# Kernel optimization log

Measured on AMD Instinct MI355X. Metric: run time of the kernel, lower is better.

Reference implementation:

```python
import jax, jax.numpy as jnp
import numpy as np

HC = 4            # hc_mult
HIDDEN = 4096
SINKHORN_ITERS = 5
HC_EPS = 1e-5
NORM_EPS = 1e-6
B, S = 2, 4096


def setup_inputs() -> dict:
    key = jax.random.key(0)
    k0, k1, k2, k3 = jax.random.split(key, 4)
    mix = (2 + HC) * HC  # 24
    return {
        "hidden_streams": jax.random.normal(k0, (B, S, HC, HIDDEN), dtype=jnp.float32),
        # small init so sigmoid/softmax gates stay in a sane range
        "fn": jax.random.normal(k1, (mix, HC * HIDDEN), dtype=jnp.float32) * 0.01,
        "base": jax.random.normal(k2, (mix,), dtype=jnp.float32),
        "scale": jax.random.normal(k3, (3,), dtype=jnp.float32),
    }


def reference(hidden_streams, fn, base, scale):
    hc = HC
    # flatten streams: [B, S, hc*hidden]
    flat = hidden_streams.reshape(hidden_streams.shape[0], hidden_streams.shape[1], -1).astype(jnp.float32)
    rsqrt = jax.lax.rsqrt(jnp.mean(jnp.square(flat), axis=-1, keepdims=True) + NORM_EPS)
    # packed projection to mix=(2+hc)*hc gate logits, RMS-scaled
    mix = jnp.einsum("bsd,md->bsm", flat, fn.astype(jnp.float32)) * rsqrt
    pre_scale, post_scale, comb_scale = scale[0], scale[1], scale[2]
    pre = jax.nn.sigmoid(mix[..., :hc] * pre_scale + base[:hc]) + HC_EPS
    post = 2.0 * jax.nn.sigmoid(mix[..., hc:2 * hc] * post_scale + base[hc:2 * hc])
    comb_logit = mix[..., 2 * hc:].reshape(*mix.shape[:-1], hc, hc) * comb_scale + base[2 * hc:].reshape(hc, hc)
    comb = jax.nn.softmax(comb_logit, axis=-1) + HC_EPS
    comb = comb / (jnp.sum(comb, axis=-2, keepdims=True) + HC_EPS)
    for _ in range(SINKHORN_ITERS - 1):
        comb = comb / (jnp.sum(comb, axis=-1, keepdims=True) + HC_EPS)
        comb = comb / (jnp.sum(comb, axis=-2, keepdims=True) + HC_EPS)
    return pre, post, comb
```

## Files before the change

### kernel.cpp

```cpp
#include <hip/hip_runtime.h>
#include <hip/hip_bf16.h>
#include <math.h>
#include <stdint.h>

#define HC 4
#define DIM 16384
#define MIXN 24
#define NROWS 8192
#define KSPLIT 16
#define KSL (DIM / KSPLIT)
#define NSTEPS (KSL / 32)
#define NSTREAM 32
#define ROWS_PER_STREAM (NROWS / NSTREAM)
#define THREADS1 512
#define NWAVE 8
#define ROWS_PER_BITER (NWAVE * 16)
#define NITER (ROWS_PER_STREAM / ROWS_PER_BITER)
#define HC_EPS 1e-5f
#define NORM_EPS 1e-6f

#define PRE_OFF 0
#define POST_OFF (NROWS * HC)
#define COMB_OFF (2 * NROWS * HC)

typedef float f32x4 __attribute__((ext_vector_type(4)));
typedef float accf4 __attribute__((ext_vector_type(4)));
typedef short bf16x8 __attribute__((ext_vector_type(8)));

__device__ __forceinline__ short f2bf(float x) {
    union { __hip_bfloat16 h; short s; } u;
    u.h = __float2bfloat16(x);
    return u.s;
}

__global__ __launch_bounds__(THREADS1) void hyper_k1(
    const float* __restrict__ hs,
    const float* __restrict__ fn,
    float* __restrict__ ws)
{
    const int tid  = threadIdx.x;
    const int wave = tid >> 6;
    const int lane = tid & 63;
    const int l15  = lane & 15;
    const int kg   = lane >> 4;
    const int ks     = blockIdx.x & (KSPLIT - 1);
    const int stream = blockIdx.x >> 4;

    __shared__ __align__(16) short s_fn[2][NSTEPS][64 * 8];

    #pragma unroll 1
    for (int p = 0; p < 8; ++p) {
        const int idx  = p * THREADS1 + tid;
        const int kgf  = idx & 3;
        const int s    = (idx >> 2) & 31;
        const int c    = (idx >> 7) & 15;
        const int tile = idx >> 11;
        const int col  = tile ? (c + 8) : c;
        const float* g = fn + (size_t)col * DIM + ks * KSL + s * 32 + kgf * 8;
        const f32x4 v0 = *(const f32x4*)g;
        const f32x4 v1 = *(const f32x4*)(g + 4);
        bf16x8 b = { f2bf(v0.x), f2bf(v0.y), f2bf(v0.z), f2bf(v0.w),
                     f2bf(v1.x), f2bf(v1.y), f2bf(v1.z), f2bf(v1.w) };
        *(bf16x8*)&s_fn[tile][s][(kgf * 16 + c) * 8] = b;
    }
    __syncthreads();

    #pragma unroll 1
    for (int it = 0; it < NITER; ++it) {
        const int rowbase = stream * ROWS_PER_STREAM + it * ROWS_PER_BITER + wave * 16;
        const float* abase = hs + (size_t)(rowbase + l15) * DIM + ks * KSL + kg * 8;

        accf4 acc0 = {0.f, 0.f, 0.f, 0.f};
        accf4 acc1 = {0.f, 0.f, 0.f, 0.f};
        accf4 accS = {0.f, 0.f, 0.f, 0.f};

        f32x4 A0, A1, B0, B1, C0, C1, D0, D1;

#define ALD(Pa, Pb, S) do { \
    const float* _a = abase + (size_t)(S) * 32; \
    Pa = *(const f32x4*)_a; Pb = *(const f32x4*)(_a + 4); \
} while (0)

#define ACP(Pa, Pb, S) do { \
    bf16x8 af = { f2bf(Pa.x), f2bf(Pa.y), f2bf(Pa.z), f2bf(Pa.w), \
                  f2bf(Pb.x), f2bf(Pb.y), f2bf(Pb.z), f2bf(Pb.w) }; \
    const bf16x8 b0 = *(const bf16x8*)&s_fn[0][S][lane * 8]; \
    const bf16x8 b1 = *(const bf16x8*)&s_fn[1][S][lane * 8]; \
    acc0 = __builtin_amdgcn_mfma_f32_16x16x32_bf16(af, b0, acc0, 0, 0, 0); \
    acc1 = __builtin_amdgcn_mfma_f32_16x16x32_bf16(af, b1, acc1, 0, 0, 0); \
    accS = __builtin_amdgcn_mfma_f32_16x16x32_bf16(af, af, accS, 0, 0, 0); \
} while (0)

        ALD(A0, A1, 0); ALD(B0, B1, 1); ALD(C0, C1, 2); ALD(D0, D1, 3);
        #pragma unroll 1
        for (int s = 0; s < NSTEPS; s += 4) {
            ACP(A0, A1, s);     if (s + 4 < NSTEPS) ALD(A0, A1, s + 4);
            ACP(B0, B1, s + 1); if (s + 5 < NSTEPS) ALD(B0, B1, s + 5);
            ACP(C0, C1, s + 2); if (s + 6 < NSTEPS) ALD(C0, C1, s + 6);
            ACP(D0, D1, s + 3); if (s + 7 < NSTEPS) ALD(D0, D1, s + 7);
        }
#undef ALD
#undef ACP

        const int rt = rowbase >> 4;
        float* w = ws + (size_t)(rt * KSPLIT + ks) * (16 * 25);
        #pragma unroll
        for (int i = 0; i < 4; ++i)
            w[(kg * 4 + i) * 25 + l15] = acc0[i];
        if (l15 >= 8) {
            #pragma unroll
            for (int i = 0; i < 4; ++i)
                w[(kg * 4 + i) * 25 + l15 + 8] = acc1[i];
        }
        #pragma unroll
        for (int i = 0; i < 4; ++i)
            if (l15 == kg * 4 + i) w[l15 * 25 + 24] = accS[i];
    }
}

__global__ __launch_bounds__(256) void hyper_k2(
    const float* __restrict__ ws,
    const float* __restrict__ base,
    const float* __restrict__ scale,
    float* __restrict__ out)
{
    const int r  = blockIdx.x * 256 + threadIdx.x;
    const int rt = r >> 4, rr = r & 15;

    float v[25];
    #pragma unroll
    for (int c = 0; c < 25; ++c) v[c] = 0.f;
    #pragma unroll 1
    for (int ks = 0; ks < KSPLIT; ++ks) {
        const float* w = ws + (size_t)(rt * KSPLIT + ks) * (16 * 25) + rr * 25;
        #pragma unroll
        for (int c = 0; c < 25; ++c) v[c] += w[c];
    }

    const float rs = 1.0f / sqrtf(v[24] * (1.0f / (float)DIM) + NORM_EPS);
    const float s0 = scale[0], s1 = scale[1], s2 = scale[2];

    #pragma unroll
    for (int i = 0; i < HC; ++i) {
        const float z = v[i] * rs * s0 + base[i];
        out[PRE_OFF + r * HC + i] = 1.0f / (1.0f + expf(-z)) + HC_EPS;
    }
    #pragma unroll
    for (int i = 0; i < HC; ++i) {
        const float z = v[HC + i] * rs * s1 + base[HC + i];
        out[POST_OFF + r * HC + i] = 2.0f / (1.0f + expf(-z));
    }

    float c[HC][HC];
    #pragma unroll
    for (int i = 0; i < HC; ++i) {
        float l[HC];
        #pragma unroll
        for (int j = 0; j < HC; ++j)
            l[j] = v[2 * HC + i * HC + j] * rs * s2 + base[2 * HC + i * HC + j];
        const float mx = fmaxf(fmaxf(l[0], l[1]), fmaxf(l[2], l[3]));
        float e[HC];
        float sum = 0.0f;
        #pragma unroll
        for (int j = 0; j < HC; ++j) { e[j] = expf(l[j] - mx); sum += e[j]; }
        const float inv = 1.0f / sum;
        #pragma unroll
        for (int j = 0; j < HC; ++j) c[i][j] = e[j] * inv + HC_EPS;
    }
    #pragma unroll
    for (int j = 0; j < HC; ++j) {
        const float cs = c[0][j] + c[1][j] + c[2][j] + c[3][j] + HC_EPS;
        const float inv = 1.0f / cs;
        c[0][j] *= inv; c[1][j] *= inv; c[2][j] *= inv; c[3][j] *= inv;
    }
    #pragma unroll
    for (int it = 0; it < 4; ++it) {
        #pragma unroll
        for (int i = 0; i < HC; ++i) {
            const float rsum = c[i][0] + c[i][1] + c[i][2] + c[i][3] + HC_EPS;
            const float inv = 1.0f / rsum;
            c[i][0] *= inv; c[i][1] *= inv; c[i][2] *= inv; c[i][3] *= inv;
        }
        #pragma unroll
        for (int j = 0; j < HC; ++j) {
            const float cs = c[0][j] + c[1][j] + c[2][j] + c[3][j] + HC_EPS;
            const float inv = 1.0f / cs;
            c[0][j] *= inv; c[1][j] *= inv; c[2][j] *= inv; c[3][j] *= inv;
        }
    }
    #pragma unroll
    for (int i = 0; i < HC; ++i)
        #pragma unroll
        for (int j = 0; j < HC; ++j)
            out[COMB_OFF + r * (HC * HC) + i * HC + j] = c[i][j];
}

extern "C" void kernel_launch(void* const* d_in, const int* in_sizes, int n_in,
                              void* d_out, int out_size, void* d_ws, size_t ws_size,
                              hipStream_t stream) {
    const float* hs    = (const float*)d_in[0];
    const float* fn    = (const float*)d_in[1];
    const float* base  = (const float*)d_in[2];
    const float* scale = (const float*)d_in[3];
    float* out = (float*)d_out;
    float* ws  = (float*)d_ws;

    hyper_k1<<<KSPLIT * NSTREAM, THREADS1, 0, stream>>>(hs, fn, ws);
    hyper_k2<<<NROWS / 256, 256, 0, stream>>>(ws, base, scale, out);
}
```

Before: 147.6 us.

## Stage activation tiles through swizzled LDS with coalesced loads and intra-block K reduction

Each block now loads whole 16-row activation tiles with fully coalesced row-contiguous float4 reads, converts them to bf16 and writes them into a double-buffered, XOR-swizzled LDS tile. The eight waves then split the K slice of that tile, run MFMAs from LDS, and reduce their partial results through a shared buffer before a single global write per tile. The goal is better DRAM access efficiency than the earlier strided per-lane loads, and overlapping the next tile's global loads with compute. The cost is extra LDS traffic, two block barriers per tile, higher LDS use that limits occupancy, and hand-written waitcnt logic.

```diff
diff --git a/kernel.cpp b/kernel.cpp
--- a/kernel.cpp
+++ b/kernel.cpp
@@ -8,14 +8,12 @@
 #define MIXN 24
 #define NROWS 8192
 #define KSPLIT 16
-#define KSL (DIM / KSPLIT)
-#define NSTEPS (KSL / 32)
+#define KSL 1024
+#define NSTEPS 32
 #define NSTREAM 32
-#define ROWS_PER_STREAM (NROWS / NSTREAM)
+#define ROWS_PER_STREAM 256
+#define NTILES 16
 #define THREADS1 512
-#define NWAVE 8
-#define ROWS_PER_BITER (NWAVE * 16)
-#define NITER (ROWS_PER_STREAM / ROWS_PER_BITER)
 #define HC_EPS 1e-5f
 #define NORM_EPS 1e-6f
 
@@ -26,6 +24,7 @@
 typedef float f32x4 __attribute__((ext_vector_type(4)));
 typedef float accf4 __attribute__((ext_vector_type(4)));
 typedef short bf16x8 __attribute__((ext_vector_type(8)));
+typedef short bf16x4 __attribute__((ext_vector_type(4)));
 
 __device__ __forceinline__ short f2bf(float x) {
     union { __hip_bfloat16 h; short s; } u;
@@ -46,7 +45,9 @@
     const int ks     = blockIdx.x & (KSPLIT - 1);
     const int stream = blockIdx.x >> 4;
 
-    __shared__ __align__(16) short s_fn[2][NSTEPS][64 * 8];
+    __shared__ __align__(16) short s_fn[2][NSTEPS][512];
+    __shared__ __align__(16) short s_a[2][NSTEPS][512];
+    __shared__ float sC[8][400];
 
     #pragma unroll 1
     for (int p = 0; p < 8; ++p) {
@@ -65,57 +66,97 @@
     }
     __syncthreads();
 
+    const int st_slo = lane >> 3;
+    const int st_kg  = (lane >> 1) & 3;
+    const int st_e   = (lane & 1) * 4;
+    const int sr0 = 2 * wave, sr1 = 2 * wave + 1;
+
+    f32x4 R0, R1, R2, R3, R4, R5, R6, R7;
+
+#define ISSUE(T) do { \
+    const float* g0 = hs + (size_t)(stream * ROWS_PER_STREAM + (T) * 16 + sr0) * DIM + ks * KSL; \
+    const float* g1 = hs + (size_t)(stream * ROWS_PER_STREAM + (T) * 16 + sr1) * DIM + ks * KSL; \
+    R0 = *(const f32x4*)(g0 +   0 + lane * 4); \
+    R1 = *(const f32x4*)(g0 + 256 + lane * 4); \
+    R2 = *(const f32x4*)(g0 + 512 + lane * 4); \
+    R3 = *(const f32x4*)(g0 + 768 + lane * 4); \
+    R4 = *(const f32x4*)(g1 +   0 + lane * 4); \
+    R5 = *(const f32x4*)(g1 + 256 + lane * 4); \
+    R6 = *(const f32x4*)(g1 + 512 + lane * 4); \
+    R7 = *(const f32x4*)(g1 + 768 + lane * 4); \
+} while (0)
+
+#define WR1(B, Rj, r, j) do { \
+    const int s_ = (j) * 8 + st_slo; \
+    int byte_ = ((s_ * 64 + st_kg * 16 + (r)) * 16) + st_e * 2; \
+    byte_ ^= ((s_ & 7) << 4); \
+    bf16x4 v_ = { f2bf(Rj.x), f2bf(Rj.y), f2bf(Rj.z), f2bf(Rj.w) }; \
+    *(bf16x4*)((char*)(&s_a[B][0][0]) + byte_) = v_; \
+} while (0)
+
+#define WRALL(B) do { \
+    WR1(B, R0, sr0, 0); WR1(B, R1, sr0, 1); WR1(B, R2, sr0, 2); WR1(B, R3, sr0, 3); \
+    WR1(B, R4, sr1, 0); WR1(B, R5, sr1, 1); WR1(B, R6, sr1, 2); WR1(B, R7, sr1, 3); \
+} while (0)
+
+    ISSUE(0);
+    asm volatile("s_waitcnt vmcnt(0)" ::: "memory");
+    WRALL(0);
+    ISSUE(1);
+
     #pragma unroll 1
-    for (int it = 0; it < NITER; ++it) {
-        const int rowbase = stream * ROWS_PER_STREAM + it * ROWS_PER_BITER + wave * 16;
-        const float* abase = hs + (size_t)(rowbase + l15) * DIM + ks * KSL + kg * 8;
+    for (int t = 0; t < NTILES; ++t) {
+        const int buf = t & 1;
+        asm volatile("s_waitcnt lgkmcnt(0)" ::: "memory");
+        __builtin_amdgcn_s_barrier();
+        __builtin_amdgcn_sched_barrier(0);
 
         accf4 acc0 = {0.f, 0.f, 0.f, 0.f};
         accf4 acc1 = {0.f, 0.f, 0.f, 0.f};
         accf4 accS = {0.f, 0.f, 0.f, 0.f};
-
-        f32x4 A0, A1, B0, B1, C0, C1, D0, D1;
-
-#define ALD(Pa, Pb, S) do { \
-    const float* _a = abase + (size_t)(S) * 32; \
-    Pa = *(const f32x4*)_a; Pb = *(const f32x4*)(_a + 4); \
-} while (0)
-
-#define ACP(Pa, Pb, S) do { \
-    bf16x8 af = { f2bf(Pa.x), f2bf(Pa.y), f2bf(Pa.z), f2bf(Pa.w), \
-                  f2bf(Pb.x), f2bf(Pb.y), f2bf(Pb.z), f2bf(Pb.w) }; \
-    const bf16x8 b0 = *(const bf16x8*)&s_fn[0][S][lane * 8]; \
-    const bf16x8 b1 = *(const bf16x8*)&s_fn[1][S][lane * 8]; \
-    acc0 = __builtin_amdgcn_mfma_f32_16x16x32_bf16(af, b0, acc0, 0, 0, 0); \
-    acc1 = __builtin_amdgcn_mfma_f32_16x16x32_bf16(af, b1, acc1, 0, 0, 0); \
-    accS = __builtin_amdgcn_mfma_f32_16x16x32_bf16(af, af, accS, 0, 0, 0); \
-} while (0)
-
-        ALD(A0, A1, 0); ALD(B0, B1, 1); ALD(C0, C1, 2); ALD(D0, D1, 3);
-        #pragma unroll 1
-        for (int s = 0; s < NSTEPS; s += 4) {
-            ACP(A0, A1, s);     if (s + 4 < NSTEPS) ALD(A0, A1, s + 4);
-            ACP(B0, B1, s + 1); if (s + 5 < NSTEPS) ALD(B0, B1, s + 5);
-            ACP(C0, C1, s + 2); if (s + 6 < NSTEPS) ALD(C0, C1, s + 6);
-            ACP(D0, D1, s + 3); if (s + 7 < NSTEPS) ALD(D0, D1, s + 7);
-        }
-#undef ALD
-#undef ACP
-
-        const int rt = rowbase >> 4;
-        float* w = ws + (size_t)(rt * KSPLIT + ks) * (16 * 25);
+        #pragma unroll
+        for (int i = 0; i < 4; ++i) {
+            const int s = wave * 4 + i;
+            int ab = ((s * 64 + lane) * 16) ^ ((s & 7) << 4);
+            const bf16x8 af = *(const bf16x8*)((const char*)(&s_a[buf][0][0]) + ab);
+            const bf16x8 b0 = *(const bf16x8*)&s_fn[0][s][lane * 8];
+            const bf16x8 b1 = *(const bf16x8*)&s_fn[1][s][lane * 8];
+            acc0 = __builtin_amdgcn_mfma_f32_16x16x32_bf16(af, b0, acc0, 0, 0, 0);
+            acc1 = __builtin_amdgcn_mfma_f32_16x16x32_bf16(af, b1, acc1, 0, 0, 0);
+            accS = __builtin_amdgcn_mfma_f32_16x16x32_bf16(af, af, accS, 0, 0, 0);
+        }
+
         #pragma unroll
         for (int i = 0; i < 4; ++i)
-            w[(kg * 4 + i) * 25 + l15] = acc0[i];
+            sC[wave][(kg * 4 + i) * 25 + l15] = acc0[i];
         if (l15 >= 8) {
             #pragma unroll
             for (int i = 0; i < 4; ++i)
-                w[(kg * 4 + i) * 25 + l15 + 8] = acc1[i];
+                sC[wave][(kg * 4 + i) * 25 + l15 + 8] = acc1[i];
         }
         #pragma unroll
         for (int i = 0; i < 4; ++i)
-            if (l15 == kg * 4 + i) w[l15 * 25 + 24] = accS[i];
-    }
+            if (l15 == kg * 4 + i) sC[wave][l15 * 25 + 24] = accS[i];
+
+        asm volatile("s_waitcnt lgkmcnt(0)" ::: "memory");
+        __builtin_amdgcn_s_barrier();
+        __builtin_amdgcn_sched_barrier(0);
+
+        if (tid < 400) {
+            const float v = sC[0][tid] + sC[1][tid] + sC[2][tid] + sC[3][tid]
+                          + sC[4][tid] + sC[5][tid] + sC[6][tid] + sC[7][tid];
+            ws[((size_t)(stream * NTILES + t) * KSPLIT + ks) * 400 + tid] = v;
+        }
+
+        if (t + 1 < NTILES) {
+            asm volatile("s_waitcnt vmcnt(1)" ::: "memory");
+            WRALL((t + 1) & 1);
+            if (t + 2 < NTILES) ISSUE(t + 2);
+        }
+    }
+#undef ISSUE
+#undef WR1
+#undef WRALL
 }
 
 __global__ __launch_bounds__(256) void hyper_k2(
@@ -132,7 +173,7 @@
     for (int c = 0; c < 25; ++c) v[c] = 0.f;
     #pragma unroll 1
     for (int ks = 0; ks < KSPLIT; ++ks) {
-        const float* w = ws + (size_t)(rt * KSPLIT + ks) * (16 * 25) + rr * 25;
+        const float* w = ws + (size_t)(rt * KSPLIT + ks) * 400 + rr * 25;
         #pragma unroll
         for (int c = 0; c < 25; ++c) v[c] += w[c];
     }
```

Result: faster. 139.2 us (-5.7%).
